# Kernel optimization log

Measured on AMD Instinct MI355X. Metric: run time of the kernel, lower is better.

The kernel has to match this reference:

```python
import jax, jax.numpy as jnp
import numpy as np
from jax import lax

DIM = 64
NUM_HEADS = 1
HEAD_DIM = DIM // NUM_HEADS
SR = 8  # reduction_ratio
SCALE = HEAD_DIM ** -0.5


def setup_inputs() -> dict:
    key = jax.random.key(0)
    ks = jax.random.split(key, 12)
    s = 0.02
    return {
        "x": jax.random.normal(ks[0], (8, 16384, DIM), dtype=jnp.float32),
        # conv sr: (out_ch, in_ch, kH, kW) torch OIHW layout
        "sr_w": jax.random.normal(ks[1], (DIM, DIM, SR, SR), dtype=jnp.float32) * s,
        "sr_b": jnp.zeros((DIM,), jnp.float32),
        "ln_g": jnp.ones((DIM,), jnp.float32),
        "ln_b": jnp.zeros((DIM,), jnp.float32),
        # torch Linear weights: (out_features, in_features)
        "q_w": jax.random.normal(ks[2], (DIM, DIM), dtype=jnp.float32) * s,
        "q_b": jnp.zeros((DIM,), jnp.float32),
        "kv_w": jax.random.normal(ks[3], (2 * DIM, DIM), dtype=jnp.float32) * s,
        "kv_b": jnp.zeros((2 * DIM,), jnp.float32),
        "proj_w": jax.random.normal(ks[4], (DIM, DIM), dtype=jnp.float32) * s,
        "proj_b": jnp.zeros((DIM,), jnp.float32),
    }


def _layernorm(x, g, b, eps=1e-5):
    mu = jnp.mean(x, axis=-1, keepdims=True)
    var = jnp.var(x, axis=-1, keepdims=True)
    return (x - mu) * lax.rsqrt(var + eps) * g + b


def reference(x, sr_w, sr_b, ln_g, ln_b, q_w, q_b, kv_w, kv_b, proj_w, proj_b):
    B, N, C = x.shape
    H = W = int(N ** 0.5)
    # q: (B, heads, N, head_dim)
    q = (x @ q_w.T + q_b).reshape(B, N, NUM_HEADS, HEAD_DIM).transpose(0, 2, 1, 3)
    # spatial reduction of KV via strided conv + LayerNorm
    x_ = x.transpose(0, 2, 1).reshape(B, C, H, W)
    x_ = lax.conv_general_dilated(
        x_, sr_w, window_strides=(SR, SR), padding="VALID",
        dimension_numbers=("NCHW", "OIHW", "NCHW"))
    x_ = x_ + sr_b[None, :, None, None]
    x_ = x_.reshape(B, C, -1).transpose(0, 2, 1)  # (B, Nr, C)
    x_ = _layernorm(x_, ln_g, ln_b)
    Nr = x_.shape[1]
    kv = (x_ @ kv_w.T + kv_b).reshape(B, Nr, 2, NUM_HEADS, HEAD_DIM)
    kv = kv.transpose(2, 0, 3, 1, 4)  # (2, B, heads, Nr, hd)
    k, v = kv[0], kv[1]
    attn = jnp.einsum("bhnd,bhmd->bhnm", q, k) * SCALE
    attn = jax.nn.softmax(attn, axis=-1)
    out = jnp.einsum("bhnm,bhmd->bhnd", attn, v)
    out = out.transpose(0, 2, 1, 3).reshape(B, N, C)
    return out @ proj_w.T + proj_b
```

## Files before the change

kernel.cpp:

```cpp
#include <hip/hip_runtime.h>
#include <hip/hip_bf16.h>


typedef __attribute__((ext_vector_type(8))) short bf16x8;
typedef __attribute__((ext_vector_type(4))) float f32x4;

__device__ __forceinline__ unsigned short f2bf(float f) {
    union { __hip_bfloat16 h; unsigned short u; } cv;
    cv.h = __hip_bfloat16(f);
    return cv.u;
}
union U8 { uint4 u; bf16x8 v; };
__device__ __forceinline__ bf16x8 pack8(float e0,float e1,float e2,float e3,
                                        float e4,float e5,float e6,float e7){
    U8 r;
    r.u.x = (unsigned)f2bf(e0) | ((unsigned)f2bf(e1)<<16);
    r.u.y = (unsigned)f2bf(e2) | ((unsigned)f2bf(e3)<<16);
    r.u.z = (unsigned)f2bf(e4) | ((unsigned)f2bf(e5)<<16);
    r.u.w = (unsigned)f2bf(e6) | ((unsigned)f2bf(e7)<<16);
    return r.v;
}
__device__ __forceinline__ bf16x8 ldg8(const unsigned short* p){
    U8 r; r.u = *(const uint4*)p; return r.v;
}

__global__ __launch_bounds__(256) void prep_kernel(
    const float* __restrict__ sr_w, const float* __restrict__ sr_b,
    const float* __restrict__ q_w, const float* __restrict__ q_b,
    const float* __restrict__ proj_w,
    unsigned short* __restrict__ wbp, float* __restrict__ conv_out,
    unsigned short* __restrict__ qwb, unsigned short* __restrict__ pwp,
    float* __restrict__ qb_s)
{
    int tid = blockIdx.x * 256 + threadIdx.x;
    {
        int i = tid & 7, n = (tid>>3)&15, g = (tid>>7)&3, ks = (tid>>9)&31,
            kc = (tid>>14)&3, w = tid>>16;
        int co = 16*w + n;
        int k  = kc*1024 + ks*32 + 8*g + i;
        int kh = k >> 9, kw = (k>>6)&7, cin = k & 63;
        wbp[tid] = f2bf(sr_w[co*4096 + cin*64 + kh*8 + kw]);
    }
    if (tid < 131072) conv_out[tid] = sr_b[tid & 63];
    if (tid < 4096)   qwb[tid] = f2bf(q_w[tid] * 0.125f);
    if (tid < 4096) {
        int i = tid & 7, g = (tid>>3)&3, s3 = (tid>>5)&1, co = tid>>6;
        int ch = 32*s3 + 16*(i>>2) + 4*g + (i&3);
        pwp[tid] = f2bf(proj_w[co*64 + ch]);
    }
    if (tid < 64) qb_s[tid] = q_b[tid] * 0.125f;
}

__global__ __launch_bounds__(256) void conv_kernel(
    const float* __restrict__ x, const unsigned short* __restrict__ wbp,
    float* __restrict__ conv_out)
{
    __shared__ char xsm[32768];
    int bid = blockIdx.x;
    int kc = bid & 3, oh = (bid>>2) & 15, b = bid >> 6;
    int t = threadIdx.x;

    const float* slab = x + ((size_t)(b*128 + oh*8 + kc*2)) * 128 * 64;
    #pragma unroll
    for (int c2 = 0; c2 < 8; ++c2) {
        int eo = (c2*256 + t) * 8;
        float4 v0 = *(const float4*)(slab + eo);
        float4 v1 = *(const float4*)(slab + eo + 4);
        int byte = eo * 2;
        int dst = byte ^ (((byte >> 10) & 7) << 4);
        U8 tmp; tmp.v = pack8(v0.x,v0.y,v0.z,v0.w,v1.x,v1.y,v1.z,v1.w);
        *(uint4*)(xsm + dst) = tmp.u;
    }
    __syncthreads();

    int w = t >> 6, lane = t & 63, g = lane >> 4, n = lane & 15;
    f32x4 acc = {0.f, 0.f, 0.f, 0.f};
    const unsigned short* wslice = wbp + (size_t)((w*4 + kc) * 32) * 512;
    int swz = (n & 7) << 4;
    #pragma unroll
    for (int ks = 0; ks < 32; ++ks) {
        bf16x8 A = ldg8(wslice + ((ks*4 + g)*16 + n) * 8);
        int byte = (ks >> 4) * 16384 + n * 1024 + ((ks & 15) * 32 + 8*g) * 2;
        U8 Bx; Bx.u = *(const uint4*)(xsm + (byte ^ swz));
        acc = __builtin_amdgcn_mfma_f32_16x16x32_bf16(A, Bx.v, acc, 0, 0, 0);
    }
    int pos = b*256 + oh*16 + n;
    int co  = 16*w + 4*g;
    #pragma unroll
    for (int r = 0; r < 4; ++r)
        atomicAdd(&conv_out[pos*64 + co + r], acc[r]);
}

__global__ __launch_bounds__(256) void lnkv_kernel(
    const float* __restrict__ conv_out,
    const float* __restrict__ ln_g, const float* __restrict__ ln_b,
    const float* __restrict__ kv_w, const float* __restrict__ kv_b,
    unsigned short* __restrict__ kbuf, unsigned short* __restrict__ vp)
{
    int wv = threadIdx.x >> 6, c = threadIdx.x & 63;
    int gblk = blockIdx.x * 4 + wv;
    int b = gblk >> 8, m = gblk & 255;
    float val = conv_out[gblk*64 + c];
    float s = val, s2 = val*val;
    #pragma unroll
    for (int o = 32; o >= 1; o >>= 1) {
        s  += __shfl_xor(s,  o, 64);
        s2 += __shfl_xor(s2, o, 64);
    }
    float mean = s * (1.f/64.f);
    float var  = s2 * (1.f/64.f) - mean*mean;
    float y = (val - mean) * rsqrtf(var + 1e-5f) * ln_g[c] + ln_b[c];
    __shared__ float ys[4][64];
    ys[wv][c] = y;
    __syncthreads();
    #pragma unroll
    for (int h = 0; h < 2; ++h) {
        int oc = c + h*64;
        float acc = kv_b[oc];
        const float* wr = kv_w + oc*64;
        #pragma unroll
        for (int j = 0; j < 64; j += 4) {
            float4 w4 = *(const float4*)(wr + j);
            acc += ys[wv][j]*w4.x + ys[wv][j+1]*w4.y + ys[wv][j+2]*w4.z + ys[wv][j+3]*w4.w;
        }
        if (h == 0) {
            kbuf[(b*256 + m)*64 + c] = f2bf(acc);
        } else {
            int ks = m >> 5, hi = (m >> 4) & 1, g2 = (m >> 2) & 3, r = m & 3;
            vp[(size_t)b*16384 + ((ks*4 + g2)*64 + c)*8 + r + 4*hi] = f2bf(acc);
        }
    }
}

__global__ __launch_bounds__(512) void attn_kernel(
    const float* __restrict__ x,
    const unsigned short* __restrict__ qwb, const float* __restrict__ qb_s,
    const unsigned short* __restrict__ kbuf, const unsigned short* __restrict__ vp,
    const unsigned short* __restrict__ pwp, const float* __restrict__ proj_b,
    float* __restrict__ out)
{
    __shared__ char Ks[32768];
    int bid = blockIdx.x;
    int b = bid >> 7, rt = bid & 127;
    int t = threadIdx.x;
    {
        const char* kb = (const char*)(kbuf + (size_t)b*16384);
        #pragma unroll
        for (int c = 0; c < 4; ++c) {
            int off = (c*512 + t) * 16;
            int dst = off ^ (((off >> 7) & 7) << 4);
            *(uint4*)(Ks + dst) = *(const uint4*)(kb + off);
        }
    }
    __syncthreads();

    int w = t >> 6, lane = t & 63, g = lane >> 4, n = lane & 15;
    int qrow = rt*128 + w*16 + n;
    const float* xr = x + ((size_t)b*16384 + qrow) * 64;
    const char* vpb = (const char*)(vp + (size_t)b*16384);

    f32x4 qacc[4];
    #pragma unroll
    for (int tau = 0; tau < 4; ++tau)
        qacc[tau] = *(const f32x4*)(qb_s + 16*tau + 4*g);
    bf16x8 xq[2];
    #pragma unroll
    for (int s = 0; s < 2; ++s) {
        float4 v0 = *(const float4*)(xr + 32*s + 8*g);
        float4 v1 = *(const float4*)(xr + 32*s + 8*g + 4);
        xq[s] = pack8(v0.x,v0.y,v0.z,v0.w,v1.x,v1.y,v1.z,v1.w);
    }
    #pragma unroll
    for (int tau = 0; tau < 4; ++tau)
        #pragma unroll
        for (int s = 0; s < 2; ++s) {
            bf16x8 A = ldg8(qwb + (16*tau + n)*64 + 32*s + 8*g);
            qacc[tau] = __builtin_amdgcn_mfma_f32_16x16x32_bf16(A, xq[s], qacc[tau], 0,0,0);
        }
    bf16x8 qkB[2];
    #pragma unroll
    for (int s2 = 0; s2 < 2; ++s2)
        qkB[s2] = pack8(qacc[2*s2][0],  qacc[2*s2][1],  qacc[2*s2][2],  qacc[2*s2][3],
                        qacc[2*s2+1][0],qacc[2*s2+1][1],qacc[2*s2+1][2],qacc[2*s2+1][3]);

    float S[16][4];
    #pragma unroll
    for (int tt = 0; tt < 16; ++tt) {
        f32x4 sa = {0.f, 0.f, 0.f, 0.f};
        int m = 16*tt + n;
        int base = m * 128;
        int swz = (m & 7) << 4;
        #pragma unroll
        for (int s2 = 0; s2 < 2; ++s2) {
            int c1 = (32*s2 + 4*g) * 2;
            uint2 d0 = *(const uint2*)(Ks + ((base + c1)      ^ swz));
            uint2 d1 = *(const uint2*)(Ks + ((base + c1 + 32) ^ swz));
            U8 A; A.u = make_uint4(d0.x, d0.y, d1.x, d1.y);
            sa = __builtin_amdgcn_mfma_f32_16x16x32_bf16(A.v, qkB[s2], sa, 0,0,0);
        }
        S[tt][0]=sa[0]; S[tt][1]=sa[1]; S[tt][2]=sa[2]; S[tt][3]=sa[3];
    }

    float rm[16];
    #pragma unroll
    for (int tt = 0; tt < 16; ++tt)
        rm[tt] = fmaxf(fmaxf(S[tt][0],S[tt][1]), fmaxf(S[tt][2],S[tt][3]));
    float m8[8];
    #pragma unroll
    for (int j = 0; j < 8; ++j) m8[j] = fmaxf(rm[2*j], rm[2*j+1]);
    float mx = fmaxf(fmaxf(fmaxf(m8[0],m8[1]),fmaxf(m8[2],m8[3])),
                     fmaxf(fmaxf(m8[4],m8[5]),fmaxf(m8[6],m8[7])));
    mx = fmaxf(mx, __shfl_xor(mx, 16, 64));
    mx = fmaxf(mx, __shfl_xor(mx, 32, 64));
    #pragma unroll
    for (int tt = 0; tt < 16; ++tt)
        #pragma unroll
        for (int r = 0; r < 4; ++r)
            S[tt][r] = __expf(S[tt][r] - mx);
    float rs[16];
    #pragma unroll
    for (int tt = 0; tt < 16; ++tt) rs[tt] = (S[tt][0]+S[tt][1]) + (S[tt][2]+S[tt][3]);
    float s8[8];
    #pragma unroll
    for (int j = 0; j < 8; ++j) s8[j] = rs[2*j] + rs[2*j+1];
    float ssum = ((s8[0]+s8[1])+(s8[2]+s8[3])) + ((s8[4]+s8[5])+(s8[6]+s8[7]));
    ssum += __shfl_xor(ssum, 16, 64);
    ssum += __shfl_xor(ssum, 32, 64);
    float inv = 1.f / ssum;

    f32x4 oacc[4] = {{0,0,0,0},{0,0,0,0},{0,0,0,0},{0,0,0,0}};
    #pragma unroll
    for (int ks = 0; ks < 8; ++ks) {
        bf16x8 Bp = pack8(S[2*ks][0],  S[2*ks][1],  S[2*ks][2],  S[2*ks][3],
                          S[2*ks+1][0],S[2*ks+1][1],S[2*ks+1][2],S[2*ks+1][3]);
        #pragma unroll
        for (int tc = 0; tc < 4; ++tc) {
            U8 A; A.u = *(const uint4*)(vpb + ((ks*4 + g)*64 + 16*tc + n) * 16);
            oacc[tc] = __builtin_amdgcn_mfma_f32_16x16x32_bf16(A.v, Bp, oacc[tc], 0,0,0);
        }
    }

    bf16x8 Bo[2];
    #pragma unroll
    for (int s3 = 0; s3 < 2; ++s3)
        Bo[s3] = pack8(oacc[2*s3][0]*inv,   oacc[2*s3][1]*inv,
                       oacc[2*s3][2]*inv,   oacc[2*s3][3]*inv,
                       oacc[2*s3+1][0]*inv, oacc[2*s3+1][1]*inv,
                       oacc[2*s3+1][2]*inv, oacc[2*s3+1][3]*inv);
    f32x4 pacc[4];
    #pragma unroll
    for (int tf = 0; tf < 4; ++tf)
        pacc[tf] = *(const f32x4*)(proj_b + 16*tf + 4*g);
    #pragma unroll
    for (int tf = 0; tf < 4; ++tf)
        #pragma unroll
        for (int s3 = 0; s3 < 2; ++s3) {
            bf16x8 Aw = ldg8(pwp + (((16*tf + n)*2 + s3)*4 + g)*8);
            pacc[tf] = __builtin_amdgcn_mfma_f32_16x16x32_bf16(Aw, Bo[s3], pacc[tf], 0,0,0);
        }
    float* orow = out + ((size_t)b*16384 + qrow) * 64;
    #pragma unroll
    for (int tf = 0; tf < 4; ++tf)
        *(float4*)(orow + 16*tf + 4*g) = *(float4*)&pacc[tf];
}

extern "C" void kernel_launch(void* const* d_in, const int* in_sizes, int n_in,
                              void* d_out, int out_size, void* d_ws, size_t ws_size,
                              hipStream_t stream)
{
    const float* x      = (const float*)d_in[0];
    const float* sr_w   = (const float*)d_in[1];
    const float* sr_b   = (const float*)d_in[2];
    const float* ln_g   = (const float*)d_in[3];
    const float* ln_b   = (const float*)d_in[4];
    const float* q_w    = (const float*)d_in[5];
    const float* q_b    = (const float*)d_in[6];
    const float* kv_w   = (const float*)d_in[7];
    const float* kv_b   = (const float*)d_in[8];
    const float* proj_w = (const float*)d_in[9];
    const float* proj_b = (const float*)d_in[10];
    float* out = (float*)d_out;

    char* wsb = (char*)d_ws;
    unsigned short* wbp  = (unsigned short*)(wsb);
    float*          conv = (float*)(wsb + 524288);
    unsigned short* kbuf = (unsigned short*)(wsb + 1048576);
    unsigned short* vp   = (unsigned short*)(wsb + 1310720);
    unsigned short* qwb  = (unsigned short*)(wsb + 1572864);
    unsigned short* pwp  = (unsigned short*)(wsb + 1581056);
    float*          qb_s = (float*)(wsb + 1589248);

    hipLaunchKernelGGL(prep_kernel, dim3(1024), dim3(256), 0, stream,
                       sr_w, sr_b, q_w, q_b, proj_w, wbp, conv, qwb, pwp, qb_s);
    hipLaunchKernelGGL(conv_kernel, dim3(512), dim3(256), 0, stream, x, wbp, conv);
    hipLaunchKernelGGL(lnkv_kernel, dim3(512), dim3(256), 0, stream,
                       conv, ln_g, ln_b, kv_w, kv_b, kbuf, vp);
    hipLaunchKernelGGL(attn_kernel, dim3(1024), dim3(512), 0, stream,
                       x, qwb, qb_s, kbuf, vp, pwp, proj_b, out);
}
```

Baseline: 158.2 us.

## Fuse strided conv with LayerNorm and KV projection, drop atomic split-K

Merges the conv and LN+KV kernels into one kernel. Each 512-thread block now owns a full output row of 16 positions and covers all of K by looping over two slabs of x. Partial sums across waves are reduced in shared memory instead of with global atomics. This removes the conv_out buffer, its bias initialisation in prep, the atomics and one kernel launch. In exchange the grid shrinks from 512 to 128 blocks, which lowers parallelism on a GPU with many CUs, and the conv phase becomes more serial.

```diff
diff --git a/kernel.cpp b/kernel.cpp
--- a/kernel.cpp
+++ b/kernel.cpp
@@ -25,10 +25,10 @@
 }
 
 __global__ __launch_bounds__(256) void prep_kernel(
-    const float* __restrict__ sr_w, const float* __restrict__ sr_b,
+    const float* __restrict__ sr_w,
     const float* __restrict__ q_w, const float* __restrict__ q_b,
     const float* __restrict__ proj_w,
-    unsigned short* __restrict__ wbp, float* __restrict__ conv_out,
+    unsigned short* __restrict__ wbp,
     unsigned short* __restrict__ qwb, unsigned short* __restrict__ pwp,
     float* __restrict__ qb_s)
 {
@@ -41,7 +41,6 @@
         int kh = k >> 9, kw = (k>>6)&7, cin = k & 63;
         wbp[tid] = f2bf(sr_w[co*4096 + cin*64 + kh*8 + kw]);
     }
-    if (tid < 131072) conv_out[tid] = sr_b[tid & 63];
     if (tid < 4096)   qwb[tid] = f2bf(q_w[tid] * 0.125f);
     if (tid < 4096) {
         int i = tid & 7, g = (tid>>3)&3, s3 = (tid>>5)&1, co = tid>>6;
@@ -51,83 +50,105 @@
     if (tid < 64) qb_s[tid] = q_b[tid] * 0.125f;
 }
 
-__global__ __launch_bounds__(256) void conv_kernel(
+__global__ __launch_bounds__(512) void convln_kernel(
     const float* __restrict__ x, const unsigned short* __restrict__ wbp,
-    float* __restrict__ conv_out)
-{
-    __shared__ char xsm[32768];
-    int bid = blockIdx.x;
-    int kc = bid & 3, oh = (bid>>2) & 15, b = bid >> 6;
-    int t = threadIdx.x;
-
-    const float* slab = x + ((size_t)(b*128 + oh*8 + kc*2)) * 128 * 64;
-    #pragma unroll
-    for (int c2 = 0; c2 < 8; ++c2) {
-        int eo = (c2*256 + t) * 8;
-        float4 v0 = *(const float4*)(slab + eo);
-        float4 v1 = *(const float4*)(slab + eo + 4);
-        int byte = eo * 2;
-        int dst = byte ^ (((byte >> 10) & 7) << 4);
-        U8 tmp; tmp.v = pack8(v0.x,v0.y,v0.z,v0.w,v1.x,v1.y,v1.z,v1.w);
-        *(uint4*)(xsm + dst) = tmp.u;
-    }
-    __syncthreads();
-
-    int w = t >> 6, lane = t & 63, g = lane >> 4, n = lane & 15;
-    f32x4 acc = {0.f, 0.f, 0.f, 0.f};
-    const unsigned short* wslice = wbp + (size_t)((w*4 + kc) * 32) * 512;
-    int swz = (n & 7) << 4;
-    #pragma unroll
-    for (int ks = 0; ks < 32; ++ks) {
-        bf16x8 A = ldg8(wslice + ((ks*4 + g)*16 + n) * 8);
-        int byte = (ks >> 4) * 16384 + n * 1024 + ((ks & 15) * 32 + 8*g) * 2;
-        U8 Bx; Bx.u = *(const uint4*)(xsm + (byte ^ swz));
-        acc = __builtin_amdgcn_mfma_f32_16x16x32_bf16(A, Bx.v, acc, 0, 0, 0);
-    }
-    int pos = b*256 + oh*16 + n;
-    int co  = 16*w + 4*g;
-    #pragma unroll
-    for (int r = 0; r < 4; ++r)
-        atomicAdd(&conv_out[pos*64 + co + r], acc[r]);
-}
-
-__global__ __launch_bounds__(256) void lnkv_kernel(
-    const float* __restrict__ conv_out,
+    const float* __restrict__ sr_b,
     const float* __restrict__ ln_g, const float* __restrict__ ln_b,
     const float* __restrict__ kv_w, const float* __restrict__ kv_b,
     unsigned short* __restrict__ kbuf, unsigned short* __restrict__ vp)
 {
-    int wv = threadIdx.x >> 6, c = threadIdx.x & 63;
-    int gblk = blockIdx.x * 4 + wv;
-    int b = gblk >> 8, m = gblk & 255;
-    float val = conv_out[gblk*64 + c];
-    float s = val, s2 = val*val;
-    #pragma unroll
-    for (int o = 32; o >= 1; o >>= 1) {
-        s  += __shfl_xor(s,  o, 64);
-        s2 += __shfl_xor(s2, o, 64);
-    }
-    float mean = s * (1.f/64.f);
-    float var  = s2 * (1.f/64.f) - mean*mean;
-    float y = (val - mean) * rsqrtf(var + 1e-5f) * ln_g[c] + ln_b[c];
-    __shared__ float ys[4][64];
-    ys[wv][c] = y;
+    __shared__ uint4 xsm4[4096];
+    char* xsm = (char*)xsm4;
+    float* red = (float*)xsm;
+    float* ysp = (float*)(xsm + 49152);
+
+    int bid = blockIdx.x;
+    int b = bid >> 4, oh = bid & 15;
+    int t = threadIdx.x;
+    int w = t >> 6, lane = t & 63, g = lane >> 4, n = lane & 15;
+
+    f32x4 acc[4] = {{0,0,0,0},{0,0,0,0},{0,0,0,0},{0,0,0,0}};
+    int khl = w >> 1;
+    int kwh = w & 1;
+
+    #pragma unroll
+    for (int p = 0; p < 2; ++p) {
+        const float* slab = x + (size_t)(b*128 + oh*8 + 4*p) * 128 * 64;
+        #pragma unroll
+        for (int c2 = 0; c2 < 8; ++c2) {
+            int eo = (c2*512 + t) * 8;
+            float4 v0 = *(const float4*)(slab + eo);
+            float4 v1 = *(const float4*)(slab + eo + 4);
+            int byte = eo * 2;
+            int dst = byte ^ (((byte >> 10) & 7) << 4);
+            U8 tmp; tmp.v = pack8(v0.x,v0.y,v0.z,v0.w,v1.x,v1.y,v1.z,v1.w);
+            *(uint4*)(xsm + dst) = tmp.u;
+        }
+        __syncthreads();
+
+        int khp = 4*p + khl;
+        int kc  = khp >> 1;
+        int swz = (n & 7) << 4;
+        #pragma unroll
+        for (int j = 0; j < 8; ++j) {
+            int ks  = (khp & 1)*16 + kwh*8 + j;
+            int kw  = kwh*4 + (j >> 1);
+            int cb  = ((j & 1) << 5) + 8*g;
+            int byte = khl*16384 + (n*8 + kw)*128 + cb*2;
+            U8 Bx; Bx.u = *(const uint4*)(xsm + (byte ^ swz));
+            #pragma unroll
+            for (int tc = 0; tc < 4; ++tc) {
+                bf16x8 A = ldg8(wbp + ((((tc*4 + kc)*32 + ks)*4 + g)*16 + n)*8);
+                acc[tc] = __builtin_amdgcn_mfma_f32_16x16x32_bf16(A, Bx.v, acc[tc], 0, 0, 0);
+            }
+        }
+        __syncthreads();
+    }
+
+    #pragma unroll
+    for (int tc = 0; tc < 4; ++tc) {
+        int byte = w*4096 + n*256 + (16*tc + 4*g)*4;
+        *(f32x4*)(xsm + (byte ^ ((n & 7) << 4))) = acc[tc];
+    }
     __syncthreads();
-    #pragma unroll
-    for (int h = 0; h < 2; ++h) {
-        int oc = c + h*64;
-        float acc = kv_b[oc];
-        const float* wr = kv_w + oc*64;
-        #pragma unroll
-        for (int j = 0; j < 64; j += 4) {
-            float4 w4 = *(const float4*)(wr + j);
-            acc += ys[wv][j]*w4.x + ys[wv][j+1]*w4.y + ys[wv][j+2]*w4.z + ys[wv][j+3]*w4.w;
-        }
-        if (h == 0) {
-            kbuf[(b*256 + m)*64 + c] = f2bf(acc);
-        } else {
-            int ks = m >> 5, hi = (m >> 4) & 1, g2 = (m >> 2) & 3, r = m & 3;
-            vp[(size_t)b*16384 + ((ks*4 + g2)*64 + c)*8 + r + 4*hi] = f2bf(acc);
+
+    int c = lane;
+    #pragma unroll
+    for (int pp = 0; pp < 2; ++pp) {
+        int pos = w + 8*pp;
+        int swzp = (pos & 7) << 4;
+        float val = sr_b[c];
+        #pragma unroll
+        for (int w8 = 0; w8 < 8; ++w8)
+            val += *(const float*)(xsm + ((w8*4096 + pos*256 + 4*c) ^ swzp));
+        float s = val, s2 = val*val;
+        #pragma unroll
+        for (int o = 32; o >= 1; o >>= 1) {
+            s  += __shfl_xor(s,  o, 64);
+            s2 += __shfl_xor(s2, o, 64);
+        }
+        float mean = s * (1.f/64.f);
+        float var  = s2 * (1.f/64.f) - mean*mean;
+        float y = (val - mean) * rsqrtf(var + 1e-5f) * ln_g[c] + ln_b[c];
+        ysp[pos*64 + c] = y;
+        int m = oh*16 + pos;
+        #pragma unroll
+        for (int h = 0; h < 2; ++h) {
+            int oc = c + h*64;
+            float a2 = kv_b[oc];
+            const float* wr = kv_w + oc*64;
+            #pragma unroll
+            for (int jj = 0; jj < 64; jj += 4) {
+                float4 w4 = *(const float4*)(wr + jj);
+                a2 += ysp[pos*64+jj]*w4.x + ysp[pos*64+jj+1]*w4.y
+                    + ysp[pos*64+jj+2]*w4.z + ysp[pos*64+jj+3]*w4.w;
+            }
+            if (h == 0) {
+                kbuf[(b*256 + m)*64 + c] = f2bf(a2);
+            } else {
+                int ks2 = m >> 5, hi = (m >> 4) & 1, g2 = (m >> 2) & 3, r = m & 3;
+                vp[(size_t)b*16384 + ((ks2*4 + g2)*64 + c)*8 + r + 4*hi] = f2bf(a2);
+            }
         }
     }
 }
@@ -283,18 +304,16 @@
 
     char* wsb = (char*)d_ws;
     unsigned short* wbp  = (unsigned short*)(wsb);
-    float*          conv = (float*)(wsb + 524288);
-    unsigned short* kbuf = (unsigned short*)(wsb + 1048576);
-    unsigned short* vp   = (unsigned short*)(wsb + 1310720);
-    unsigned short* qwb  = (unsigned short*)(wsb + 1572864);
-    unsigned short* pwp  = (unsigned short*)(wsb + 1581056);
-    float*          qb_s = (float*)(wsb + 1589248);
+    unsigned short* kbuf = (unsigned short*)(wsb + 524288);
+    unsigned short* vp   = (unsigned short*)(wsb + 786432);
+    unsigned short* qwb  = (unsigned short*)(wsb + 1048576);
+    unsigned short* pwp  = (unsigned short*)(wsb + 1056768);
+    float*          qb_s = (float*)(wsb + 1064960);
 
     hipLaunchKernelGGL(prep_kernel, dim3(1024), dim3(256), 0, stream,
-                       sr_w, sr_b, q_w, q_b, proj_w, wbp, conv, qwb, pwp, qb_s);
-    hipLaunchKernelGGL(conv_kernel, dim3(512), dim3(256), 0, stream, x, wbp, conv);
-    hipLaunchKernelGGL(lnkv_kernel, dim3(512), dim3(256), 0, stream,
-                       conv, ln_g, ln_b, kv_w, kv_b, kbuf, vp);
+                       sr_w, q_w, q_b, proj_w, wbp, qwb, pwp, qb_s);
+    hipLaunchKernelGGL(convln_kernel, dim3(128), dim3(512), 0, stream,
+                       x, wbp, sr_b, ln_g, ln_b, kv_w, kv_b, kbuf, vp);
     hipLaunchKernelGGL(attn_kernel, dim3(1024), dim3(512), 0, stream,
                        x, qwb, qb_s, kbuf, vp, pwp, proj_b, out);
 }
```

After: 175.2 us. 1.11x slower.
